# Performance work log

Measured on AMD Instinct MI355X. Metric: run time of the kernel, lower is better.

Reference implementation:

```python
import jax, jax.numpy as jnp
import numpy as np

B, T, S, D, V = 32, 2048, 256, 1024, 56
STAR_PENALTY = -1.0
NEG = -1e30  # -inf surrogate that is safe for gradients


def setup_inputs() -> dict:
    key = jax.random.key(0)
    k1, k2, k3 = jax.random.split(key, 3)
    features = jax.random.normal(k1, (B, T, D), jnp.float32)
    targets = jax.random.randint(k2, (B, S), 1, V)  # 0 is the blank; labels in [1, V)
    W = jax.random.normal(k3, (V, D), jnp.float32) * (1.0 / 32.0)  # 1/sqrt(D)
    b = jnp.zeros((V,), jnp.float32)
    input_lengths = jnp.full((B,), T, jnp.int32)
    target_lengths = jnp.full((B,), S, jnp.int32)
    return dict(features=features, W=W, b=b, targets=targets,
                input_lengths=input_lengths, target_lengths=target_lengths)


def _star_ctc_losses(logp, targets, input_lengths, target_lengths, star_penalty):
    """Star-CTC forward (DP) score.
    logp: (T, N, C) log-softmax emissions; targets: (N, S) labels (blank=0 excluded).
    Extended state sequence [*, t1, *, t2, ..., tS, *]: star states play the role of
    CTC blanks but act as penalized wildcards, emitting logsumexp(logp)+star_penalty
    (== star_penalty for normalized log-probs). Standard CTC transition topology:
    self-loop, advance by 1, advance by 2 into a token state when it differs from the
    previous token. Returns per-sequence negative log-likelihood, shape (N,)."""
    Tlen, N, C = logp.shape
    Slen = targets.shape[1]
    L = 2 * Slen + 1
    ext = jnp.zeros((N, L), targets.dtype).at[:, 1::2].set(targets)  # (N, L)
    is_star = (jnp.arange(L) % 2 == 0)[None, :]                      # (1, L)
    prev2 = jnp.pad(ext[:, :-2], ((0, 0), (2, 0)), constant_values=-1)
    allow_skip = (~is_star) & (ext != prev2)                         # (N, L)

    def emit(logp_t):  # logp_t: (N, C) -> (N, L)
        star_e = star_penalty + jax.nn.logsumexp(logp_t, axis=-1, keepdims=True)
        tok_e = jnp.take_along_axis(logp_t, ext, axis=-1)
        return jnp.where(is_star, star_e, tok_e)

    alpha0 = jnp.where(jnp.arange(L)[None, :] < 2, emit(logp[0]), NEG)

    def step(alpha, xs):
        logp_t, t = xs
        a1 = jnp.pad(alpha[:, :-1], ((0, 0), (1, 0)), constant_values=NEG)
        a2 = jnp.where(allow_skip,
                       jnp.pad(alpha[:, :-2], ((0, 0), (2, 0)), constant_values=NEG),
                       NEG)
        new = jnp.logaddexp(jnp.logaddexp(alpha, a1), a2) + emit(logp_t)
        new = jnp.where(t < input_lengths[:, None], new, alpha)  # freeze past input_length
        return new, None

    alpha, _ = jax.lax.scan(step, alpha0, (logp[1:], jnp.arange(1, Tlen)))
    last = 2 * target_lengths                  # index of the final star state
    rows = jnp.arange(N)
    score = jnp.logaddexp(alpha[rows, last], alpha[rows, last - 1])
    return -score


def reference(features, W, b, targets, input_lengths, target_lengths):
    # classifier + log_softmax (Dropout(0.2) is identity at eval time)
    logits = jnp.einsum('btd,vd->btv', features, W) + b
    logp = jax.nn.log_softmax(logits.astype(jnp.float32), axis=-1)
    logp = jnp.transpose(logp, (1, 0, 2))      # (T, N, C) as in logits.permute(1,0,2)
    losses = _star_ctc_losses(logp, targets, input_lengths, target_lengths, STAR_PENALTY)
    # ctc_reduce_mean: length-normalized mean loss
    return jnp.mean(losses / target_lengths.astype(losses.dtype))
```

## Files before the change

kernel.cpp:

```cpp
#include <hip/hip_runtime.h>
#include <hip/hip_bf16.h>
#include <math.h>

typedef __attribute__((ext_vector_type(4))) float f32x4;
typedef __attribute__((ext_vector_type(8))) short s16x8;

#define LOG2E 1.4426950408889634f
#define LN2f  0.6931471805599453f
#define INV_E 0.36787944117144233f

__device__ __forceinline__ short bfc(float x) {
  unsigned u = __float_as_uint(x);
  unsigned r = u + 0x7fffu + ((u >> 16) & 1u);
  return (short)(r >> 16);
}

__device__ __forceinline__ unsigned pk2(float x, float y) {
  union { __hip_bfloat162 h; unsigned u; } c;
  c.h = __float22bfloat162_rn(make_float2(x, y));
  return c.u;
}

__device__ __forceinline__ float bperm(float v, int byte_addr) {
  return __int_as_float(__builtin_amdgcn_ds_bpermute(byte_addr, __float_as_int(v)));
}

__device__ __forceinline__ float rdlane(float v, int lane) {
  return __int_as_float(__builtin_amdgcn_readlane(__float_as_int(v), lane));
}

__device__ __forceinline__ float pick9(int j, float a0, float a1, float a2,
                                       float a3, float a4, float a5, float a6,
                                       float a7, float a8) {
  float v = a0;
  if (j == 1) v = a1;
  if (j == 2) v = a2;
  if (j == 3) v = a3;
  if (j == 4) v = a4;
  if (j == 5) v = a5;
  if (j == 6) v = a6;
  if (j == 7) v = a7;
  if (j == 8) v = a8;
  return v;
}

__device__ __forceinline__ void gload_lds16(const float* g, float* l) {
  __builtin_amdgcn_global_load_lds(
      (const __attribute__((address_space(1))) unsigned int*)g,
      (__attribute__((address_space(3))) unsigned int*)l, 16, 0, 0);
}

__global__ void conv_w(const float* __restrict__ W, short* __restrict__ Wb,
                       int V, int D, int* __restrict__ flags, int nflags) {
  int idx = blockIdx.x * blockDim.x + threadIdx.x;
  if (idx < nflags) flags[idx] = 0;
  if (idx >= 64 * D) return;
  int row = idx / D, col = idx - row * D;
  Wb[idx] = (row < V) ? bfc(W[(size_t)row * D + col]) : (short)0;
}

__global__ __launch_bounds__(256) void fused_gemm_star(
    const float* __restrict__ feat, const short* __restrict__ Wb,
    const float* __restrict__ bias, float* __restrict__ pt,
    int* __restrict__ flags,
    const int* __restrict__ targets, const int* __restrict__ in_len,
    const int* __restrict__ tgt_len, float* __restrict__ partial,
    int nrows, int D, int V, int T, int S, int B, int CPB) {

  __shared__ __align__(16) float Ap[4 * 32 * 128];

  if ((int)blockIdx.x >= B) {
    const int NPROD = gridDim.x - B;
    const int NTILES = B * CPB;
    const int lane = threadIdx.x & 63;
    const int wave = threadIdx.x >> 6;
    const int m_lo = lane & 15;
    const int q = lane >> 4;
    float* wpan = Ap + wave * 32 * 128;
    char* wpanb = (char*)wpan;

    for (int i = blockIdx.x - B; i < NTILES; i += NPROD) {
      const int c = i / B;
      const int b = i - c * B;
      const int tc0 = c * 128;
      const int rlen = (T - tc0 < 128) ? (T - tc0) : 128;
      const int rowlim = b * T + tc0 + rlen;
      const int rowbase = b * T + tc0 + wave * 32;

      f32x4 acc[2][4];
      #pragma unroll
      for (int g = 0; g < 2; ++g)
        #pragma unroll
        for (int ni = 0; ni < 4; ++ni) acc[g][ni] = (f32x4){0.f, 0.f, 0.f, 0.f};

      const int xl = (lane & 31) * 16;
      const int rhalf = lane >> 5;

      for (int k0 = 0; k0 < D; k0 += 128) {
        #pragma unroll
        for (int ii = 0; ii < 16; ++ii) {
          int rl = ii * 2 + rhalf;
          int grow = rowbase + rl;
          if (grow >= nrows) grow = nrows - 1;
          int off = xl ^ ((rl & 7) << 4);
          gload_lds16(feat + (size_t)grow * D + k0 + (off >> 2),
                      wpan + ii * 256);
        }
        asm volatile("s_waitcnt vmcnt(0)" ::: "memory");
        const int l0 = m_lo, l1 = m_lo + 16;
        const int sz0 = (l0 & 7) << 4;
        #pragma unroll
        for (int kk = 0; kk < 4; ++kk) {
          int boff = kk * 128 + q * 32;
          float4 lo0 = *(const float4*)(wpanb + l0 * 512 + ((boff) ^ sz0));
          float4 hi0 = *(const float4*)(wpanb + l0 * 512 + ((boff + 16) ^ sz0));
          float4 lo1 = *(const float4*)(wpanb + l1 * 512 + ((boff) ^ sz0));
          float4 hi1 = *(const float4*)(wpanb + l1 * 512 + ((boff + 16) ^ sz0));
          const short* Bpp = Wb + (size_t)m_lo * D + k0 + kk * 32 + q * 8;
          s16x8 b0 = *(const s16x8*)(Bpp);
          s16x8 b1 = *(const s16x8*)(Bpp + (size_t)16 * D);
          s16x8 b2 = *(const s16x8*)(Bpp + (size_t)32 * D);
          s16x8 b3 = *(const s16x8*)(Bpp + (size_t)48 * D);
          union { s16x8 v; unsigned u[4]; } av0, av1;
          av0.u[0] = pk2(lo0.x, lo0.y); av0.u[1] = pk2(lo0.z, lo0.w);
          av0.u[2] = pk2(hi0.x, hi0.y); av0.u[3] = pk2(hi0.z, hi0.w);
          av1.u[0] = pk2(lo1.x, lo1.y); av1.u[1] = pk2(lo1.z, lo1.w);
          av1.u[2] = pk2(hi1.x, hi1.y); av1.u[3] = pk2(hi1.z, hi1.w);
          acc[0][0] = __builtin_amdgcn_mfma_f32_16x16x32_bf16(av0.v, b0, acc[0][0], 0, 0, 0);
          acc[0][1] = __builtin_amdgcn_mfma_f32_16x16x32_bf16(av0.v, b1, acc[0][1], 0, 0, 0);
          acc[0][2] = __builtin_amdgcn_mfma_f32_16x16x32_bf16(av0.v, b2, acc[0][2], 0, 0, 0);
          acc[0][3] = __builtin_amdgcn_mfma_f32_16x16x32_bf16(av0.v, b3, acc[0][3], 0, 0, 0);
          acc[1][0] = __builtin_amdgcn_mfma_f32_16x16x32_bf16(av1.v, b0, acc[1][0], 0, 0, 0);
          acc[1][1] = __builtin_amdgcn_mfma_f32_16x16x32_bf16(av1.v, b1, acc[1][1], 0, 0, 0);
          acc[1][2] = __builtin_amdgcn_mfma_f32_16x16x32_bf16(av1.v, b2, acc[1][2], 0, 0, 0);
          acc[1][3] = __builtin_amdgcn_mfma_f32_16x16x32_bf16(av1.v, b3, acc[1][3], 0, 0, 0);
        }
      }

      float bias_v[4];
      #pragma unroll
      for (int ni = 0; ni < 4; ++ni) {
        int col = ni * 16 + m_lo;
        bias_v[ni] = (col < V) ? bias[col] : 0.f;
      }

      #pragma unroll
      for (int g = 0; g < 2; ++g) {
        #pragma unroll
        for (int r = 0; r < 4; ++r) {
          int grow = rowbase + g * 16 + q * 4 + r;
          float lg[4];
          #pragma unroll
          for (int ni = 0; ni < 4; ++ni) {
            int col = ni * 16 + m_lo;
            lg[ni] = (col < V) ? (acc[g][ni][r] + bias_v[ni]) : -1e30f;
          }
          float m = fmaxf(fmaxf(lg[0], lg[1]), fmaxf(lg[2], lg[3]));
          #pragma unroll
          for (int off = 1; off < 16; off <<= 1) m = fmaxf(m, __shfl_xor(m, off));
          float p[4];
          #pragma unroll
          for (int ni = 0; ni < 4; ++ni) p[ni] = exp2f((lg[ni] - m) * LOG2E);
          float s = (p[0] + p[1]) + (p[2] + p[3]);
          #pragma unroll
          for (int off = 1; off < 16; off <<= 1) s += __shfl_xor(s, off);

          if (grow < rowlim) {
            float* orow = pt + (size_t)grow * 64;
            orow[m_lo] = p[0];
            orow[16 + m_lo] = p[1];
            orow[32 + m_lo] = p[2];
            if (m_lo < 8)       orow[48 + m_lo] = p[3];
            else if (m_lo == 8) orow[56] = logf(s);
            else if (m_lo == 9) orow[57] = s * INV_E;
            else                orow[48 + m_lo] = 0.f;
          }
        }
      }

      __syncthreads();
      if (threadIdx.x == 0)
        __hip_atomic_store(&flags[b * CPB + c], 1, __ATOMIC_RELEASE,
                           __HIP_MEMORY_SCOPE_AGENT);
    }
    return;
  }

  if (threadIdx.x >= 64) return;
  const int n = blockIdx.x;
  const int lane = threadIdx.x;
  const float* row = pt + (size_t)n * T * 64;
  const int len = in_len[n];
  const int tl = tgt_len[n];
  const int* tg = targets + (size_t)n * S;
  const int* fl = flags + n * CPB;

  int cdone = -1;
#define WAITC(cc)                                                            \
  do {                                                                       \
    int _c = (cc);                                                           \
    if (cdone < _c) {                                                        \
      while (cdone < _c) {                                                   \
        if (__hip_atomic_load((int*)&fl[cdone + 1], __ATOMIC_RELAXED,        \
                              __HIP_MEMORY_SCOPE_AGENT))                     \
          ++cdone;                                                           \
        else                                                                 \
          __builtin_amdgcn_s_sleep(2);                                       \
      }                                                                      \
      __builtin_amdgcn_fence(__ATOMIC_ACQUIRE, "agent");                     \
    }                                                                        \
  } while (0)

  const int s0 = lane * 4;
  int lab1 = (s0     < S) ? tg[s0]     : 0;
  int lab3 = (s0 + 1 < S) ? tg[s0 + 1] : 0;
  int lab5 = (s0 + 2 < S) ? tg[s0 + 2] : 0;
  int lab7 = (s0 + 3 < S) ? tg[s0 + 3] : 0;
  int labm1 = __shfl_up(lab7, 1);
  int labm3 = __shfl_up(lab5, 1);
  const bool sk1 = (lane > 0) && (lab1 != labm1);
  const bool sk3 = (lab3 != lab1);
  const bool sk5 = (lab5 != lab3);
  const bool sk7 = (lab7 != lab5);
  const bool skm1 = (labm1 != labm3);
  const int ad1 = lab1 << 2, ad3 = lab3 << 2, ad5 = lab5 << 2, ad7 = lab7 << 2;
  const int adm1 = labm1 << 2;

  float a0 = 0, a1 = 0, a2 = 0, a3 = 0, a4 = 0, a5 = 0, a6 = 0, a7 = 0, a8 = 0;
  float m1 = 0.f, m2 = 0.f, m3 = 0.f;
  int eps = 0, eL = 0;
  bool act = (lane == 0);

#define ROWL(t) row[(size_t)(((t) < len) ? (t) : (len - 1)) * 64 + lane]

  WAITC(0);

  float rc = row[lane];
  {
    float star = rdlane(rc, 57);
    float e1i = bperm(rc, ad1);
    if (lane == 0) { a0 = star; a1 = e1i; }
  }
  float ksum = rc;

  float rr0 = ROWL(1), rr1 = ROWL(2), rr2 = ROWL(3), rr3 = ROWL(4);
  float rr4 = ROWL(5), rr5 = ROWL(6), rr6 = ROWL(7), rr7 = ROWL(8);

  float es0v = rdlane(rr0, 57);
  float e1a = bperm(rr0, ad1), e3a = bperm(rr0, ad3);
  float e5a = bperm(rr0, ad5), e7a = bperm(rr0, ad7);
  float em1a = bperm(rr0, adm1);
  float es1v = rdlane(rr1, 57);
  float e1b = bperm(rr1, ad1), e3b = bperm(rr1, ad3);
  float e5b = bperm(rr1, ad5), e7b = bperm(rr1, ad7);

#define RENORM()                                                             \
  do {                                                                       \
    float mx = fmaxf(fmaxf(fmaxf(a0, a1), fmaxf(a2, a3)),                    \
                     fmaxf(fmaxf(a4, a5), fmaxf(a6, a7)));                   \
    mx = fmaxf(mx, a8);                                                      \
    int e = (int)((__float_as_uint(mx) >> 23) & 255) - 126;                  \
    e = (act && mx > 0.f) ? e : 0;                                           \
    a0 = ldexpf(a0, -e); a1 = ldexpf(a1, -e); a2 = ldexpf(a2, -e);           \
    a3 = ldexpf(a3, -e); a4 = ldexpf(a4, -e); a5 = ldexpf(a5, -e);           \
    a6 = ldexpf(a6, -e); a7 = ldexpf(a7, -e); a8 = ldexpf(a8, -e);           \
    eps += e;                                                                \
  } while (0)

#define PAIR(C0, C1, N0, N1, P0, P1, DOREN)                                  \
  do {                                                                       \
    ksum += C0; ksum += C1;                                                  \
    if (!act) eps = eL;                                                      \
    bool inc = (lane != 0) &&                                                \
               ((m1 != 0.f) || (m2 != 0.f) || (m3 != 0.f));                  \
    int d = inc ? (eL - eps) : 0;                                            \
    if (__builtin_expect(d > 24, 0)) {                  \
      a0 = ldexpf(a0, -d); a1 = ldexpf(a1, -d); a2 = ldexpf(a2, -d);         \
      a3 = ldexpf(a3, -d); a4 = ldexpf(a4, -d); a5 = ldexpf(a5, -d);         \
      a6 = ldexpf(a6, -d); a7 = ldexpf(a7, -d); a8 = ldexpf(a8, -d);         \
      eps += d;                                      \
    } else {                                                                 \
      m1 = ldexpf(m1, d); m2 = ldexpf(m2, d); m3 = ldexpf(m3, d);            \
    }                                                                        \
    act = act || (m1 != 0.f) || (m2 != 0.f) || (m3 != 0.f);                  \
                  \
    a8 = (a8 + a7) * es0v;                                                   \
    a7 = (a7 + a6 + (sk7 ? a5 : 0.f)) * e7a;                                 \
    a6 = (a6 + a5) * es0v;                                                   \
    a5 = (a5 + a4 + (sk5 ? a3 : 0.f)) * e5a;                                 \
    a4 = (a4 + a3) * es0v;                                                   \
    a3 = (a3 + a2 + (sk3 ? a1 : 0.f)) * e3a;                                 \
    a2 = (a2 + a1) * es0v;                                                   \
    a1 = (a1 + a0 + (sk1 ? m1 : 0.f)) * e1a;                                 \
    a0 = (a0 + m1) * es0v;                                                   \
    m1 = (m1 + m2 + (skm1 ? m3 : 0.f)) * em1a;                               \
                                                             \
    a8 = (a8 + a7) * es1v;                                                   \
    a7 = (a7 + a6 + (sk7 ? a5 : 0.f)) * e7b;                                 \
    a6 = (a6 + a5) * es1v;                                                   \
    a5 = (a5 + a4 + (sk5 ? a3 : 0.f)) * e5b;                                 \
    a4 = (a4 + a3) * es1v;                                                   \
    a3 = (a3 + a2 + (sk3 ? a1 : 0.f)) * e3b;                                 \
    a2 = (a2 + a1) * es1v;                                                   \
    a1 = (a1 + a0 + (sk1 ? m1 : 0.f)) * e1b;                                 \
    a0 = (a0 + m1) * es1v;                                                   \
    C0 = ROWL(P0); C1 = ROWL(P1);                     \
    if (DOREN) RENORM();                                                     \
      \
    es0v = rdlane(N0, 57);                                                   \
    e1a = bperm(N0, ad1); e3a = bperm(N0, ad3);                              \
    e5a = bperm(N0, ad5); e7a = bperm(N0, ad7);                              \
    em1a = bperm(N0, adm1);                                                  \
    es1v = rdlane(N1, 57);                                                   \
    e1b = bperm(N1, ad1); e3b = bperm(N1, ad3);                              \
    e5b = bperm(N1, ad5); e7b = bperm(N1, ad7);                              \
                          \
    m3 = __shfl_up(a5, 1); m2 = __shfl_up(a6, 1); m1 = __shfl_up(a7, 1);     \
    eL = __shfl_up(eps, 1);                                                  \
    if (lane == 0) { m1 = 0.f; m2 = 0.f; m3 = 0.f; }                         \
  } while (0)

  int t0 = 1;
  for (; t0 + 8 <= len; t0 += 8) {
    int tmax = t0 + 15;
    if (tmax > len - 1) tmax = len - 1;
    WAITC(tmax >> 7);
    PAIR(rr0, rr1, rr2, rr3, t0 + 8,  t0 + 9,  false);
    PAIR(rr2, rr3, rr4, rr5, t0 + 10, t0 + 11, false);
    PAIR(rr4, rr5, rr6, rr7, t0 + 12, t0 + 13, false);
    PAIR(rr6, rr7, rr0, rr1, t0 + 14, t0 + 15, true);
  }

  WAITC((len - 1) >> 7);

  for (int t = t0; t < len; ++t) {
    float cur = ROWL(t);
    float esv = rdlane(cur, 57);
    float e1v = bperm(cur, ad1), e3v = bperm(cur, ad3);
    float e5v = bperm(cur, ad5), e7v = bperm(cur, ad7);
    ksum += cur;
    if (!act) eps = eL;
    bool inc = (lane != 0) && (m1 != 0.f);
    int d = inc ? (eL - eps) : 0;
    float m1s;
    if (__builtin_expect(d > 24, 0)) {
      a0 = ldexpf(a0, -d); a1 = ldexpf(a1, -d); a2 = ldexpf(a2, -d);
      a3 = ldexpf(a3, -d); a4 = ldexpf(a4, -d); a5 = ldexpf(a5, -d);
      a6 = ldexpf(a6, -d); a7 = ldexpf(a7, -d); a8 = ldexpf(a8, -d);
      eps += d; m1s = m1;
    } else {
      m1s = inc ? ldexpf(m1, d) : 0.f;
    }
    act = act || (m1s != 0.f);
    a8 = (a8 + a7) * esv;
    a7 = (a7 + a6 + (sk7 ? a5 : 0.f)) * e7v;
    a6 = (a6 + a5) * esv;
    a5 = (a5 + a4 + (sk5 ? a3 : 0.f)) * e5v;
    a4 = (a4 + a3) * esv;
    a3 = (a3 + a2 + (sk3 ? a1 : 0.f)) * e3v;
    a2 = (a2 + a1) * esv;
    a1 = (a1 + a0 + (sk1 ? m1s : 0.f)) * e1v;
    a0 = (a0 + m1s) * esv;
    if ((t & 7) == 0) RENORM();
    m1 = __shfl_up(a7, 1);
    eL = __shfl_up(eps, 1);
    if (lane == 0) m1 = 0.f;
  }

  int last = 2 * tl;
  int kx = last >> 3, jx = last & 7;
  if (kx > 63) { kx = 63; jx = last - 504; }
  int ky = (last - 1) >> 3, jy = (last - 1) & 7;
  float vx = pick9(jx, a0, a1, a2, a3, a4, a5, a6, a7, a8);
  float vy = pick9(jy, a0, a1, a2, a3, a4, a5, a6, a7, a8);
  float k56 = __shfl(ksum, 56);
  float sx = __shfl(vx, kx); int ex = __shfl(eps, kx);
  float sy = __shfl(vy, ky); int ey = __shfl(eps, ky);
  if (lane == 0) {
    int em = (ex > ey) ? ex : ey;
    float v = ldexpf(sx, ex - em) + ldexpf(sy, ey - em);
    float score = logf(v) + (float)em * LN2f - k56;
    partial[n] = -score / (float)tl;
  }
#undef WAITC
#undef ROWL
#undef RENORM
#undef PAIR
}

__global__ void reduce_mean(const float* __restrict__ partial,
                            float* __restrict__ out, int B) {
  float v = 0.f;
  for (int i = threadIdx.x; i < B; i += 64) v += partial[i];
  #pragma unroll
  for (int off = 32; off > 0; off >>= 1) v += __shfl_down(v, off, 64);
  if (threadIdx.x == 0) out[0] = v / (float)B;
}

extern "C" void kernel_launch(void* const* d_in, const int* in_sizes, int n_in,
                              void* d_out, int out_size, void* d_ws, size_t ws_size,
                              hipStream_t stream) {
  const float* feat = (const float*)d_in[0];
  const float* W = (const float*)d_in[1];
  const float* bias = (const float*)d_in[2];
  const int* targets = (const int*)d_in[3];
  const int* in_len = (const int*)d_in[4];
  const int* tgt_len = (const int*)d_in[5];
  float* out = (float*)d_out;

  const int V = in_sizes[2];
  const int D = in_sizes[1] / V;
  const int B = in_sizes[4];
  const int T = in_sizes[0] / (B * D);
  const int S = in_sizes[3] / B;
  const int nrows = B * T;

  float* pt = (float*)d_ws;
  float* partial = pt + (size_t)nrows * 64;
  short* Wb = (short*)(partial + B);
  const int CPB = (T + 127) / 128;
  int* flags = (int*)((char*)Wb + (size_t)64 * D * sizeof(short));

  conv_w<<<(64 * D + 255) / 256, 256, 0, stream>>>(W, Wb, V, D,
                                                   flags, B * CPB);

  const int NTILES = B * CPB;
  int NPROD = 128;
  if (NPROD > NTILES) NPROD = NTILES;
  fused_gemm_star<<<dim3(B + NPROD), 256, 0, stream>>>(
      feat, Wb, bias, pt, flags, targets, in_len, tgt_len, partial,
      nrows, D, V, T, S, B, CPB);

  reduce_mean<<<1, 64, 0, stream>>>(partial, out, B);
}
```

Measured before the change: 670.7 us.

## Split CTC alpha recursion across two wavefronts with LDS boundary exchange

The per-sequence DP recursion is now spread over two 64-lane wavefronts, each lane holding 5 states instead of 9, with a boundary exchange between the waves through shared memory and __syncthreads every step. Surplus waves in the block just match the barrier count and exit. The aim is to shorten the serial per-step dependency chain by halving per-lane work. In exchange every timestep now pays a block barrier plus LDS traffic, which could cost more than the arithmetic it saves.

```diff
diff --git a/kernel.cpp b/kernel.cpp
--- a/kernel.cpp
+++ b/kernel.cpp
@@ -29,18 +29,13 @@
   return __int_as_float(__builtin_amdgcn_readlane(__float_as_int(v), lane));
 }
 
-__device__ __forceinline__ float pick9(int j, float a0, float a1, float a2,
-                                       float a3, float a4, float a5, float a6,
-                                       float a7, float a8) {
-  float v = a0;
-  if (j == 1) v = a1;
-  if (j == 2) v = a2;
-  if (j == 3) v = a3;
-  if (j == 4) v = a4;
-  if (j == 5) v = a5;
-  if (j == 6) v = a6;
-  if (j == 7) v = a7;
-  if (j == 8) v = a8;
+__device__ __forceinline__ float pick5(int j, float x0, float x1, float x2,
+                                       float x3, float x4) {
+  float v = x0;
+  if (j == 1) v = x1;
+  if (j == 2) v = x2;
+  if (j == 3) v = x3;
+  if (j == 4) v = x4;
   return v;
 }
 
@@ -186,14 +181,28 @@
     return;
   }
 
-  if (threadIdx.x >= 64) return;
   const int n = blockIdx.x;
-  const int lane = threadIdx.x;
+  const int wid = threadIdx.x >> 6;
+  const int lane = threadIdx.x & 63;
+  const int len = in_len[n];
+
+  if (wid >= 2) {
+    int t0e = 1;
+    for (; t0e + 8 <= len; t0e += 8) {
+      __syncthreads(); __syncthreads(); __syncthreads(); __syncthreads();
+    }
+    for (int t = t0e; t < len; ++t) __syncthreads();
+    __syncthreads();
+    return;
+  }
+
+  const int g = wid * 64 + lane;
   const float* row = pt + (size_t)n * T * 64;
-  const int len = in_len[n];
   const int tl = tgt_len[n];
   const int* tg = targets + (size_t)n * S;
   const int* fl = flags + n * CPB;
+  float* bnd = Ap;
+  float* fin = Ap + 16;
 
   int cdone = -1;
 #define WAITC(cc)                                                            \
@@ -211,25 +220,21 @@
     }                                                                        \
   } while (0)
 
-  const int s0 = lane * 4;
-  int lab1 = (s0     < S) ? tg[s0]     : 0;
-  int lab3 = (s0 + 1 < S) ? tg[s0 + 1] : 0;
-  int lab5 = (s0 + 2 < S) ? tg[s0 + 2] : 0;
-  int lab7 = (s0 + 3 < S) ? tg[s0 + 3] : 0;
-  int labm1 = __shfl_up(lab7, 1);
-  int labm3 = __shfl_up(lab5, 1);
-  const bool sk1 = (lane > 0) && (lab1 != labm1);
-  const bool sk3 = (lab3 != lab1);
-  const bool sk5 = (lab5 != lab3);
-  const bool sk7 = (lab7 != lab5);
+  const int jA = 2 * g, jB = 2 * g + 1;
+  const int labA  = (jA < S) ? tg[jA] : 0;
+  const int labB  = (jB < S) ? tg[jB] : 0;
+  const int labm1 = (g > 0 && jA - 1 < S) ? tg[jA - 1] : 0;
+  const int labm3 = (g > 0 && jA - 2 < S) ? tg[jA - 2] : 0;
+  const bool sk1  = (g > 0) && (labA != labm1);
+  const bool sk3  = (labB != labA);
   const bool skm1 = (labm1 != labm3);
-  const int ad1 = lab1 << 2, ad3 = lab3 << 2, ad5 = lab5 << 2, ad7 = lab7 << 2;
-  const int adm1 = labm1 << 2;
-
-  float a0 = 0, a1 = 0, a2 = 0, a3 = 0, a4 = 0, a5 = 0, a6 = 0, a7 = 0, a8 = 0;
+  const int adA = labA << 2, adB = labB << 2, adm1 = labm1 << 2;
+
+  float b0 = 0, b1v = 0, b2v = 0, b3v = 0, b4v = 0;
   float m1 = 0.f, m2 = 0.f, m3 = 0.f;
   int eps = 0, eL = 0;
-  bool act = (lane == 0);
+  bool act = (g == 0);
+  int pp = 0;
 
 #define ROWL(t) row[(size_t)(((t) < len) ? (t) : (len - 1)) * 64 + lane]
 
@@ -238,8 +243,8 @@
   float rc = row[lane];
   {
     float star = rdlane(rc, 57);
-    float e1i = bperm(rc, ad1);
-    if (lane == 0) { a0 = star; a1 = e1i; }
+    float e1i = bperm(rc, adA);
+    if (g == 0) { b0 = star; b1v = e1i; }
   }
   float ksum = rc;
 
@@ -247,23 +252,17 @@
   float rr4 = ROWL(5), rr5 = ROWL(6), rr6 = ROWL(7), rr7 = ROWL(8);
 
   float es0v = rdlane(rr0, 57);
-  float e1a = bperm(rr0, ad1), e3a = bperm(rr0, ad3);
-  float e5a = bperm(rr0, ad5), e7a = bperm(rr0, ad7);
-  float em1a = bperm(rr0, adm1);
+  float eAa = bperm(rr0, adA), eBa = bperm(rr0, adB), em1a = bperm(rr0, adm1);
   float es1v = rdlane(rr1, 57);
-  float e1b = bperm(rr1, ad1), e3b = bperm(rr1, ad3);
-  float e5b = bperm(rr1, ad5), e7b = bperm(rr1, ad7);
+  float eAb = bperm(rr1, adA), eBb = bperm(rr1, adB);
 
 #define RENORM()                                                             \
   do {                                                                       \
-    float mx = fmaxf(fmaxf(fmaxf(a0, a1), fmaxf(a2, a3)),                    \
-                     fmaxf(fmaxf(a4, a5), fmaxf(a6, a7)));                   \
-    mx = fmaxf(mx, a8);                                                      \
+    float mx = fmaxf(fmaxf(fmaxf(b0, b1v), fmaxf(b2v, b3v)), b4v);           \
     int e = (int)((__float_as_uint(mx) >> 23) & 255) - 126;                  \
     e = (act && mx > 0.f) ? e : 0;                                           \
-    a0 = ldexpf(a0, -e); a1 = ldexpf(a1, -e); a2 = ldexpf(a2, -e);           \
-    a3 = ldexpf(a3, -e); a4 = ldexpf(a4, -e); a5 = ldexpf(a5, -e);           \
-    a6 = ldexpf(a6, -e); a7 = ldexpf(a7, -e); a8 = ldexpf(a8, -e);           \
+    b0 = ldexpf(b0, -e); b1v = ldexpf(b1v, -e); b2v = ldexpf(b2v, -e);       \
+    b3v = ldexpf(b3v, -e); b4v = ldexpf(b4v, -e);                            \
     eps += e;                                                                \
   } while (0)
 
@@ -271,53 +270,51 @@
   do {                                                                       \
     ksum += C0; ksum += C1;                                                  \
     if (!act) eps = eL;                                                      \
-    bool inc = (lane != 0) &&                                                \
+    bool inc = (g != 0) &&                                                   \
                ((m1 != 0.f) || (m2 != 0.f) || (m3 != 0.f));                  \
     int d = inc ? (eL - eps) : 0;                                            \
     if (__builtin_expect(d > 24, 0)) {                  \
-      a0 = ldexpf(a0, -d); a1 = ldexpf(a1, -d); a2 = ldexpf(a2, -d);         \
-      a3 = ldexpf(a3, -d); a4 = ldexpf(a4, -d); a5 = ldexpf(a5, -d);         \
-      a6 = ldexpf(a6, -d); a7 = ldexpf(a7, -d); a8 = ldexpf(a8, -d);         \
+      b0 = ldexpf(b0, -d); b1v = ldexpf(b1v, -d); b2v = ldexpf(b2v, -d);     \
+      b3v = ldexpf(b3v, -d); b4v = ldexpf(b4v, -d);                          \
       eps += d;                                      \
     } else {                                                                 \
       m1 = ldexpf(m1, d); m2 = ldexpf(m2, d); m3 = ldexpf(m3, d);            \
     }                                                                        \
     act = act || (m1 != 0.f) || (m2 != 0.f) || (m3 != 0.f);                  \
                   \
-    a8 = (a8 + a7) * es0v;                                                   \
-    a7 = (a7 + a6 + (sk7 ? a5 : 0.f)) * e7a;                                 \
-    a6 = (a6 + a5) * es0v;                                                   \
-    a5 = (a5 + a4 + (sk5 ? a3 : 0.f)) * e5a;                                 \
-    a4 = (a4 + a3) * es0v;                                                   \
-    a3 = (a3 + a2 + (sk3 ? a1 : 0.f)) * e3a;                                 \
-    a2 = (a2 + a1) * es0v;                                                   \
-    a1 = (a1 + a0 + (sk1 ? m1 : 0.f)) * e1a;                                 \
-    a0 = (a0 + m1) * es0v;                                                   \
-    m1 = (m1 + m2 + (skm1 ? m3 : 0.f)) * em1a;                               \
+    b4v = (b4v + b3v) * es0v;                                                \
+    b3v = (b3v + b2v + (sk3 ? b1v : 0.f)) * eBa;                             \
+    b2v = (b2v + b1v) * es0v;                                                \
+    b1v = (b1v + b0 + (sk1 ? m1 : 0.f)) * eAa;                               \
+    b0  = (b0 + m1) * es0v;                                                  \
+    m1  = (m1 + m2 + (skm1 ? m3 : 0.f)) * em1a;                              \
                                                              \
-    a8 = (a8 + a7) * es1v;                                                   \
-    a7 = (a7 + a6 + (sk7 ? a5 : 0.f)) * e7b;                                 \
-    a6 = (a6 + a5) * es1v;                                                   \
-    a5 = (a5 + a4 + (sk5 ? a3 : 0.f)) * e5b;                                 \
-    a4 = (a4 + a3) * es1v;                                                   \
-    a3 = (a3 + a2 + (sk3 ? a1 : 0.f)) * e3b;                                 \
-    a2 = (a2 + a1) * es1v;                                                   \
-    a1 = (a1 + a0 + (sk1 ? m1 : 0.f)) * e1b;                                 \
-    a0 = (a0 + m1) * es1v;                                                   \
+    b4v = (b4v + b3v) * es1v;                                                \
+    b3v = (b3v + b2v + (sk3 ? b1v : 0.f)) * eBb;                             \
+    b2v = (b2v + b1v) * es1v;                                                \
+    b1v = (b1v + b0 + (sk1 ? m1 : 0.f)) * eAb;                               \
+    b0  = (b0 + m1) * es1v;                                                  \
     C0 = ROWL(P0); C1 = ROWL(P1);                     \
     if (DOREN) RENORM();                                                     \
-      \
+            \
     es0v = rdlane(N0, 57);                                                   \
-    e1a = bperm(N0, ad1); e3a = bperm(N0, ad3);                              \
-    e5a = bperm(N0, ad5); e7a = bperm(N0, ad7);                              \
-    em1a = bperm(N0, adm1);                                                  \
+    eAa = bperm(N0, adA); eBa = bperm(N0, adB); em1a = bperm(N0, adm1);      \
     es1v = rdlane(N1, 57);                                                   \
-    e1b = bperm(N1, ad1); e3b = bperm(N1, ad3);                              \
-    e5b = bperm(N1, ad5); e7b = bperm(N1, ad7);                              \
-                          \
-    m3 = __shfl_up(a5, 1); m2 = __shfl_up(a6, 1); m1 = __shfl_up(a7, 1);     \
+    eAb = bperm(N1, adA); eBb = bperm(N1, adB);                              \
+                                    \
+    m3 = __shfl_up(b1v, 1); m2 = __shfl_up(b2v, 1); m1 = __shfl_up(b3v, 1);  \
     eL = __shfl_up(eps, 1);                                                  \
-    if (lane == 0) { m1 = 0.f; m2 = 0.f; m3 = 0.f; }                         \
+    if (wid == 0 && lane == 63) {                   \
+      float* sl = bnd + pp * 8;                                              \
+      sl[0] = b1v; sl[1] = b2v; sl[2] = b3v; ((int*)sl)[3] = eps;            \
+    }                                                                        \
+    __syncthreads();                                                         \
+    if (wid == 1 && lane == 0) {                                             \
+      const float* sl = bnd + pp * 8;                                        \
+      m3 = sl[0]; m2 = sl[1]; m1 = sl[2]; eL = ((const int*)sl)[3];          \
+    }                                                                        \
+    if (g == 0) { m1 = 0.f; m2 = 0.f; m3 = 0.f; }                            \
+    pp ^= 1;                                                                 \
   } while (0)
 
   int t0 = 1;
@@ -336,47 +333,54 @@
   for (int t = t0; t < len; ++t) {
     float cur = ROWL(t);
     float esv = rdlane(cur, 57);
-    float e1v = bperm(cur, ad1), e3v = bperm(cur, ad3);
-    float e5v = bperm(cur, ad5), e7v = bperm(cur, ad7);
+    float eAv = bperm(cur, adA), eBv = bperm(cur, adB);
     ksum += cur;
     if (!act) eps = eL;
-    bool inc = (lane != 0) && (m1 != 0.f);
+    bool inc = (g != 0) && (m1 != 0.f);
     int d = inc ? (eL - eps) : 0;
     float m1s;
     if (__builtin_expect(d > 24, 0)) {
-      a0 = ldexpf(a0, -d); a1 = ldexpf(a1, -d); a2 = ldexpf(a2, -d);
-      a3 = ldexpf(a3, -d); a4 = ldexpf(a4, -d); a5 = ldexpf(a5, -d);
-      a6 = ldexpf(a6, -d); a7 = ldexpf(a7, -d); a8 = ldexpf(a8, -d);
+      b0 = ldexpf(b0, -d); b1v = ldexpf(b1v, -d); b2v = ldexpf(b2v, -d);
+      b3v = ldexpf(b3v, -d); b4v = ldexpf(b4v, -d);
       eps += d; m1s = m1;
     } else {
       m1s = inc ? ldexpf(m1, d) : 0.f;
     }
     act = act || (m1s != 0.f);
-    a8 = (a8 + a7) * esv;
-    a7 = (a7 + a6 + (sk7 ? a5 : 0.f)) * e7v;
-    a6 = (a6 + a5) * esv;
-    a5 = (a5 + a4 + (sk5 ? a3 : 0.f)) * e5v;
-    a4 = (a4 + a3) * esv;
-    a3 = (a3 + a2 + (sk3 ? a1 : 0.f)) * e3v;
-    a2 = (a2 + a1) * esv;
-    a1 = (a1 + a0 + (sk1 ? m1s : 0.f)) * e1v;
-    a0 = (a0 + m1s) * esv;
+    b4v = (b4v + b3v) * esv;
+    b3v = (b3v + b2v + (sk3 ? b1v : 0.f)) * eBv;
+    b2v = (b2v + b1v) * esv;
+    b1v = (b1v + b0 + (sk1 ? m1s : 0.f)) * eAv;
+    b0  = (b0 + m1s) * esv;
     if ((t & 7) == 0) RENORM();
-    m1 = __shfl_up(a7, 1);
+    m1 = __shfl_up(b3v, 1);
     eL = __shfl_up(eps, 1);
-    if (lane == 0) m1 = 0.f;
+    if (wid == 0 && lane == 63) {
+      float* sl = bnd + pp * 8;
+      sl[2] = b3v; ((int*)sl)[3] = eps;
+    }
+    __syncthreads();
+    if (wid == 1 && lane == 0) {
+      const float* sl = bnd + pp * 8;
+      m1 = sl[2]; eL = ((const int*)sl)[3];
+    }
+    if (g == 0) m1 = 0.f;
+    pp ^= 1;
   }
 
   int last = 2 * tl;
-  int kx = last >> 3, jx = last & 7;
-  if (kx > 63) { kx = 63; jx = last - 504; }
-  int ky = (last - 1) >> 3, jy = (last - 1) & 7;
-  float vx = pick9(jx, a0, a1, a2, a3, a4, a5, a6, a7, a8);
-  float vy = pick9(jy, a0, a1, a2, a3, a4, a5, a6, a7, a8);
-  float k56 = __shfl(ksum, 56);
-  float sx = __shfl(vx, kx); int ex = __shfl(eps, kx);
-  float sy = __shfl(vy, ky); int ey = __shfl(eps, ky);
-  if (lane == 0) {
+  int gx = last >> 2, jx = last & 3;
+  if (gx > 127) { gx = 127; jx = last - 508; }
+  int gy = (last - 1) >> 2, jy = (last - 1) & 3;
+  float vx = pick5(jx, b0, b1v, b2v, b3v, b4v);
+  float vy = pick5(jy, b0, b1v, b2v, b3v, b4v);
+  if (g == gx) { fin[0] = vx; ((int*)fin)[1] = eps; }
+  if (g == gy) { fin[2] = vy; ((int*)fin)[3] = eps; }
+  __syncthreads();
+  if (g == 0) {
+    float k56 = rdlane(ksum, 56);
+    float sx = fin[0]; int ex = ((const int*)fin)[1];
+    float sy = fin[2]; int ey = ((const int*)fin)[3];
     int em = (ex > ey) ? ex : ey;
     float v = ldexpf(sx, ex - em) + ldexpf(sy, ey - em);
     float score = logf(v) + (float)em * LN2f - k56;
```

Result: no change. 679.5 us (+1.3%).
